# Optimization experiments

Hardware: AMD Instinct MI355X
Metric: run time of the kernel (lower is better)

Reference implementation:

```python
import jax, jax.numpy as jnp
import numpy as np

N, P, K = 2048, 32, 20000

def _log_normal(x, m, s):
    return -0.5 * jnp.log(2.0 * jnp.pi * s * s) - (x - m) ** 2 / (2.0 * s * s)

def setup_inputs() -> dict:
    key = jax.random.key(0)
    k1, k2, k3, k4 = jax.random.split(key, 4)
    X = jax.random.normal(k1, (N, P), dtype=jnp.float32)
    Y = jax.random.randint(k2, (N, K), 0, 100, dtype=jnp.int32)
    mu = jax.random.normal(k3, (K,), dtype=jnp.float32)
    beta = jax.random.normal(k4, (P, K), dtype=jnp.float32)
    m0 = jnp.float32(0.0)
    s0 = jnp.float32(1.0)
    return {"X": X, "Y": Y, "mu": mu, "beta": beta, "m0": m0, "s0": s0}

def reference(X, Y, mu, beta, m0, s0):
    # logits: [N, K]
    logits = mu + jnp.matmul(X, beta)
    # log softmax == log(pi) where pi = exp(logits - logsumexp)
    logp = jax.nn.log_softmax(logits, axis=1)
    Yf = Y.astype(logits.dtype)
    n = jnp.sum(Yf, axis=1)  # total counts per sample
    # sum over samples of multinomial log-pmf:
    #   lgamma(n+1) - sum_j lgamma(y_j+1) + sum_j y_j * log(pi_j)
    log_lik = (jnp.sum(jax.lax.lgamma(n + 1.0))
               - jnp.sum(jax.lax.lgamma(Yf + 1.0))
               + jnp.sum(Yf * logp))
    log_prior = jnp.sum(_log_normal(mu, m0, s0)) + jnp.sum(_log_normal(beta, m0, s0))
    return jnp.reshape(log_lik + log_prior, (1,))
```

## Files before the change

kernel.cpp:

```cpp
#include <hip/hip_runtime.h>
#include <math.h>

#define NROWS 2048
#define KDIM  20000
#define PDIM  32
#define CHW   80
#define SLOTS 20
#define PADW  84
#define KSL   24
#define RGRP  32
#define MAINB (RGRP * KSL)
#define PREPB 313
#define PRIORB 64
#define STATS_N (NROWS * 4)

#define OFF_STATS (KDIM * PDIM * 2)
#define OFF_PRIOR (OFF_STATS + STATS_N * 4)
#define WS_NEEDED (OFF_PRIOR + PREPB * 8)

typedef short bf16x8 __attribute__((ext_vector_type(8)));
typedef unsigned short u16x8 __attribute__((ext_vector_type(8)));
typedef float f32x4  __attribute__((ext_vector_type(4)));
typedef int   i32x4  __attribute__((ext_vector_type(4)));

__device__ __forceinline__ short f2bf(float f) {
  unsigned u = __float_as_uint(f);
  u += 0x7FFF + ((u >> 16) & 1);
  return (short)(u >> 16);
}
__device__ __forceinline__ float wredf(float v) {
#pragma unroll
  for (int o = 32; o > 0; o >>= 1) v += __shfl_down(v, o, 64);
  return v;
}
__device__ __forceinline__ double wredd(double v) {
#pragma unroll
  for (int o = 32; o > 0; o >>= 1) v += __shfl_down(v, o, 64);
  return v;
}


__global__ void prep_k(const float* __restrict__ beta, const float* __restrict__ mu,
                       const float* __restrict__ m0p, const float* __restrict__ s0p,
                       unsigned short* __restrict__ betaT,
                       float* __restrict__ stats, double* __restrict__ priorpart)
{
  __shared__ float red[4];
  const int tid = threadIdx.x;
  const int gi = blockIdx.x * 256 + tid;
  if (gi < STATS_N) stats[gi] = 0.0f;

  const int kk = blockIdx.x * 64 + (tid & 63);
  const int pg = tid >> 6;
  const float m0 = m0p[0], s0 = s0p[0];
  const float inv2s2 = 0.5f / (s0 * s0);
  const float cnst = -0.5f * logf(6.283185307179586f * s0 * s0);

  float fs = 0.0f;
  if (kk < KDIM) {
    u16x8 w;
#pragma unroll
    for (int i = 0; i < 8; ++i) {
      float v = beta[(pg * 8 + i) * KDIM + kk];
      float d = v - m0;
      fs += cnst - d * d * inv2s2;
      w[i] = (unsigned short)f2bf(v);
    }
    *(u16x8*)(betaT + kk * PDIM + pg * 8) = w;
    if (pg == 0) {
      float d = mu[kk] - m0;
      fs += cnst - d * d * inv2s2;
    }
  }
  fs = wredf(fs);
  if ((tid & 63) == 0) red[tid >> 6] = fs;
  __syncthreads();
  if (tid == 0)
    priorpart[blockIdx.x] =
        (double)red[0] + (double)red[1] + (double)red[2] + (double)red[3];
}

__global__ __launch_bounds__(256, 3) void main_k(
    const float* __restrict__ X, const int* __restrict__ Y,
    const float* __restrict__ mu, const unsigned short* __restrict__ betaT,
    float* __restrict__ stats)
{
  __shared__ float lgt[128];
  __shared__ int ybuf[2][64 * PADW];
  const int tid = threadIdx.x;
  if (tid < 128) lgt[tid] = lgammaf((float)tid + 1.0f);

  const int rg = blockIdx.x / KSL;
  const int ks = blockIdx.x % KSL;
  const int sbase = rg * 64;
  const int cstart = (ks < 10) ? ks * 11 : 110 + (ks - 10) * 10;
  const int cps    = (ks < 10) ? 11 : 10;

  const int wave = tid >> 6, lane = tid & 63;
  const int lg = lane >> 4, ln = lane & 15;

  int goff[5], loff[5];
#pragma unroll
  for (int i = 0; i < 5; ++i) {
    const int flat = i * 64 + lane;
    const int rowl = flat / SLOTS, slot = flat % SLOTS;
    const int row = wave * 16 + rowl;
    goff[i] = (sbase + row) * KDIM + slot * 4;
    loff[i] = row * PADW + slot * 4;
  }

  const int samp = sbase + wave * 16 + ln;
  bf16x8 xb;
  {
    const float* xp = X + samp * PDIM + lg * 8;
    float4 x0 = *(const float4*)xp;
    float4 x1 = *(const float4*)(xp + 4);
    xb[0] = f2bf(x0.x); xb[1] = f2bf(x0.y); xb[2] = f2bf(x0.z); xb[3] = f2bf(x0.w);
    xb[4] = f2bf(x1.x); xb[5] = f2bf(x1.y); xb[6] = f2bf(x1.z); xb[7] = f2bf(x1.w);
  }

  float S = 0.f, SY = 0.f, SYL = 0.f, SLG = 0.f;

#define GLOAD(c_) do { const int _cb = (c_) * CHW;                            \
    r0 = *(const i32x4*)(Y + goff[0] + _cb);                                  \
    r1 = *(const i32x4*)(Y + goff[1] + _cb);                                  \
    r2 = *(const i32x4*)(Y + goff[2] + _cb);                                  \
    r3 = *(const i32x4*)(Y + goff[3] + _cb);                                  \
    r4 = *(const i32x4*)(Y + goff[4] + _cb);                                  \
  } while (0)
#define DSW(b_) do {                                                          \
    *(i32x4*)&ybuf[b_][loff[0]] = r0;                                         \
    *(i32x4*)&ybuf[b_][loff[1]] = r1;                                         \
    *(i32x4*)&ybuf[b_][loff[2]] = r2;                                         \
    *(i32x4*)&ybuf[b_][loff[3]] = r3;                                         \
    *(i32x4*)&ybuf[b_][loff[4]] = r4;                                         \
  } while (0)

  i32x4 r0, r1, r2, r3, r4;
  GLOAD(cstart);
  DSW(0);
  GLOAD(cstart + 1);
  __syncthreads();

  const int ybase = wave * 16 + ln;

  for (int ch = 0; ch < cps; ++ch) {
    const int cur = ch & 1;
    const int cbase = (cstart + ch) * CHW;
#pragma unroll
    for (int tt = 0; tt < 5; ++tt) {
      i32x4 yv = *(const i32x4*)&ybuf[cur][ybase * PADW + (tt * 4 + lg) * 4];
      bf16x8 af = *(const bf16x8*)(betaT + (cbase + tt * 16 + ln) * PDIM + lg * 8);
      float4 m4 = *(const float4*)(mu + cbase + tt * 16 + lg * 4);
      f32x4 cc = { m4.x, m4.y, m4.z, m4.w };
      cc = __builtin_amdgcn_mfma_f32_16x16x32_bf16(af, xb, cc, 0, 0, 0);
      const int ya[4] = { yv[0], yv[1], yv[2], yv[3] };
#pragma unroll
      for (int j = 0; j < 4; ++j) {
        const float logit = cc[j];
        S += __expf(logit);
        const float yf = (float)ya[j];
        SY += yf;
        SYL = fmaf(yf, logit, SYL);
        SLG += lgt[ya[j]];
      }
    }
    if (ch + 1 < cps) {
      DSW(cur ^ 1);
      if (ch + 2 < cps) GLOAD(cstart + ch + 2);
    }
  }
#undef GLOAD
#undef DSW

  S   += __shfl_xor(S,   16, 64); S   += __shfl_xor(S,   32, 64);
  SY  += __shfl_xor(SY,  16, 64); SY  += __shfl_xor(SY,  32, 64);
  SYL += __shfl_xor(SYL, 16, 64); SYL += __shfl_xor(SYL, 32, 64);
  SLG += __shfl_xor(SLG, 16, 64); SLG += __shfl_xor(SLG, 32, 64);
  if (lg == 0) {
    atomicAdd(&stats[samp * 4 + 0], S);
    atomicAdd(&stats[samp * 4 + 1], SY);
    atomicAdd(&stats[samp * 4 + 2], SYL);
    atomicAdd(&stats[samp * 4 + 3], SLG);
  }
}

__global__ void combine_k(const float* __restrict__ stats,
                          const double* __restrict__ priorpart,
                          float* __restrict__ out)
{
  double part = 0.0;
  for (int r = threadIdx.x; r < NROWS; r += 256) {
    float S   = stats[r * 4 + 0];
    float n   = stats[r * 4 + 1];
    float SYL = stats[r * 4 + 2];
    float SLG = stats[r * 4 + 3];
    part += (double)lgammaf(n + 1.0f) - (double)SLG + (double)SYL
          - (double)n * (double)logf(S);
  }
  for (int i = threadIdx.x; i < PREPB; i += 256) part += priorpart[i];
  part = wredd(part);
  __shared__ double pd[4];
  if ((threadIdx.x & 63) == 0) pd[threadIdx.x >> 6] = part;
  __syncthreads();
  if (threadIdx.x == 0)
    out[0] = (float)(pd[0] + pd[1] + pd[2] + pd[3]);
}


__global__ void fb_init_k(float* stats, double* acc) {
  int i = blockIdx.x * blockDim.x + threadIdx.x;
  if (i < STATS_N) stats[i] = 0.0f;
  if (i == 0) acc[0] = 0.0;
}

__global__ __launch_bounds__(256, 8) void fb_main_k(
    const float* __restrict__ X, const int* __restrict__ Y,
    const float* __restrict__ mu, const float* __restrict__ beta,
    const float* __restrict__ m0p, const float* __restrict__ s0p,
    float* __restrict__ stats, double* __restrict__ acc)
{
  __shared__ float lgt[128];
  __shared__ float red[4];
  const int tid = threadIdx.x;
  const int FB_MAINB = 2048;

  if (blockIdx.x >= FB_MAINB) {
    const int b = blockIdx.x - FB_MAINB;
    const float m0 = m0p[0], s0 = s0p[0];
    const float inv2s2 = 0.5f / (s0 * s0);
    const float cnst = -0.5f * logf(6.283185307179586f * s0 * s0);
    const int total = KDIM + PDIM * KDIM;
    float fs = 0.0f;
    for (int i = b * 256 + tid; i < total; i += PRIORB * 256) {
      float v = (i < KDIM) ? mu[i] : beta[i - KDIM];
      float d = v - m0;
      fs += cnst - d * d * inv2s2;
    }
    fs = wredf(fs);
    if ((tid & 63) == 0) red[tid >> 6] = fs;
    __syncthreads();
    if (tid == 0) {
      double tsum = (double)red[0] + (double)red[1] + (double)red[2] + (double)red[3];
      atomicAdd(acc, tsum);
    }
    return;
  }

  const int brow  = blockIdx.x / 64;
  const int chunk = blockIdx.x % 64;
  const int wave = tid >> 6;
  const int lane = tid & 63;
  const int lg = lane >> 4;
  const int ln = lane & 15;
  const int sample = brow * 64 + wave * 16 + ln;

  if (tid < 128) lgt[tid] = lgammaf((float)tid + 1.0f);
  __syncthreads();

  bf16x8 xb;
  {
    const float* xp = X + sample * PDIM + lg * 8;
    float4 x0 = *(const float4*)xp;
    float4 x1 = *(const float4*)(xp + 4);
    xb[0] = f2bf(x0.x); xb[1] = f2bf(x0.y); xb[2] = f2bf(x0.z); xb[3] = f2bf(x0.w);
    xb[4] = f2bf(x1.x); xb[5] = f2bf(x1.y); xb[6] = f2bf(x1.z); xb[7] = f2bf(x1.w);
  }
  const size_t ybase = (size_t)sample * KDIM + (size_t)lg * 4;
  const float* bcol = beta + lg * 8 * KDIM + ln;

  float S = 0.f, SY = 0.f, SYL = 0.f, SLG = 0.f;
  int t = chunk;
  const int FB_NTILE = 1250;
  int4   yv = *(const int4*)(Y + ybase + (size_t)t * 16);
  float4 m4 = *(const float4*)(mu + t * 16 + lg * 4);

  while (t < FB_NTILE) {
    const int col0 = t * 16;
    const int tn = t + 64;
    const int ts = (tn < FB_NTILE) ? tn : t;
    int4   yv_n = *(const int4*)(Y + ybase + (size_t)ts * 16);
    float4 m4_n = *(const float4*)(mu + ts * 16 + lg * 4);
    bf16x8 af;
#pragma unroll
    for (int i = 0; i < 8; ++i) af[i] = f2bf(bcol[i * KDIM + col0]);
    f32x4 c = { m4.x, m4.y, m4.z, m4.w };
    c = __builtin_amdgcn_mfma_f32_16x16x32_bf16(af, xb, c, 0, 0, 0);
    const int ya[4] = { yv.x, yv.y, yv.z, yv.w };
#pragma unroll
    for (int j = 0; j < 4; ++j) {
      const float logit = c[j];
      S += __expf(logit);
      const float yf = (float)ya[j];
      SY  += yf;
      SYL += yf * logit;
      SLG += lgt[ya[j]];
    }
    t = tn; yv = yv_n; m4 = m4_n;
  }

  S   += __shfl_xor(S,   16, 64); S   += __shfl_xor(S,   32, 64);
  SY  += __shfl_xor(SY,  16, 64); SY  += __shfl_xor(SY,  32, 64);
  SYL += __shfl_xor(SYL, 16, 64); SYL += __shfl_xor(SYL, 32, 64);
  SLG += __shfl_xor(SLG, 16, 64); SLG += __shfl_xor(SLG, 32, 64);
  if (lg == 0) {
    atomicAdd(&stats[sample * 4 + 0], S);
    atomicAdd(&stats[sample * 4 + 1], SY);
    atomicAdd(&stats[sample * 4 + 2], SYL);
    atomicAdd(&stats[sample * 4 + 3], SLG);
  }
}

__global__ void fb_combine_k(const float* __restrict__ stats,
                             const double* __restrict__ acc,
                             float* __restrict__ out)
{
  double part = 0.0;
  for (int r = threadIdx.x; r < NROWS; r += 256) {
    float S   = stats[r * 4 + 0];
    float n   = stats[r * 4 + 1];
    float SYL = stats[r * 4 + 2];
    float SLG = stats[r * 4 + 3];
    part += (double)lgammaf(n + 1.0f) - (double)SLG + (double)SYL
          - (double)n * (double)logf(S);
  }
  part = wredd(part);
  __shared__ double pd[4];
  if ((threadIdx.x & 63) == 0) pd[threadIdx.x >> 6] = part;
  __syncthreads();
  if (threadIdx.x == 0)
    out[0] = (float)(pd[0] + pd[1] + pd[2] + pd[3] + acc[0]);
}

extern "C" void kernel_launch(void* const* d_in, const int* in_sizes, int n_in,
                              void* d_out, int out_size, void* d_ws, size_t ws_size,
                              hipStream_t stream) {
  const float* X    = (const float*)d_in[0];
  const int*   Y    = (const int*)d_in[1];
  const float* mu   = (const float*)d_in[2];
  const float* beta = (const float*)d_in[3];
  const float* m0   = (const float*)d_in[4];
  const float* s0   = (const float*)d_in[5];
  float* out = (float*)d_out;

  if (ws_size >= (size_t)WS_NEEDED) {
    unsigned short* betaT = (unsigned short*)d_ws;
    float*  stats = (float*)((char*)d_ws + OFF_STATS);
    double* prior = (double*)((char*)d_ws + OFF_PRIOR);
    prep_k<<<dim3(PREPB), dim3(256), 0, stream>>>(beta, mu, m0, s0, betaT, stats, prior);
    main_k<<<dim3(MAINB), dim3(256), 0, stream>>>(X, Y, mu, betaT, stats);
    combine_k<<<dim3(1), dim3(256), 0, stream>>>(stats, prior, out);
  } else {
    float*  stats = (float*)d_ws;
    double* acc   = (double*)((char*)d_ws + STATS_N * sizeof(float));
    fb_init_k<<<dim3((STATS_N + 255) / 256), dim3(256), 0, stream>>>(stats, acc);
    fb_main_k<<<dim3(2048 + PRIORB), dim3(256), 0, stream>>>(
        X, Y, mu, beta, m0, s0, stats, acc);
    fb_combine_k<<<dim3(1), dim3(256), 0, stream>>>(stats, acc, out);
  }
}
```

Measured before the change: 44.84 us.

## Deepen Y prefetch to two register sets and fuse combine via last-block counter

The Y tile loads now use two register sets, so the global load for chunk ch+2 is issued at the start of iteration ch and overlaps a full chunk of MFMA and exp work. Previously it was issued after the LDS store at the end of the iteration. The separate single-block combine kernel is removed: a completion counter reset in prep_k lets the last main_k block do the final reduction, saving one launch. The cost is more live VGPRs, which may hurt occupancy under launch_bounds(256,3), plus a threadfence and an atomic in every block.

Result: slower. 107.1 us (+138.9%).

```diff
diff --git a/kernel.cpp b/kernel.cpp
--- a/kernel.cpp
+++ b/kernel.cpp
@@ -16,7 +16,8 @@
 
 #define OFF_STATS (KDIM * PDIM * 2)
 #define OFF_PRIOR (OFF_STATS + STATS_N * 4)
-#define WS_NEEDED (OFF_PRIOR + PREPB * 8)
+#define OFF_CNT   (OFF_PRIOR + PREPB * 8)
+#define WS_NEEDED (OFF_CNT + 16)
 
 typedef short bf16x8 __attribute__((ext_vector_type(8)));
 typedef unsigned short u16x8 __attribute__((ext_vector_type(8)));
@@ -43,12 +44,14 @@
 __global__ void prep_k(const float* __restrict__ beta, const float* __restrict__ mu,
                        const float* __restrict__ m0p, const float* __restrict__ s0p,
                        unsigned short* __restrict__ betaT,
-                       float* __restrict__ stats, double* __restrict__ priorpart)
+                       float* __restrict__ stats, double* __restrict__ priorpart,
+                       unsigned* __restrict__ counter)
 {
   __shared__ float red[4];
   const int tid = threadIdx.x;
   const int gi = blockIdx.x * 256 + tid;
   if (gi < STATS_N) stats[gi] = 0.0f;
+  if (gi == 0) counter[0] = 0u;
 
   const int kk = blockIdx.x * 64 + (tid & 63);
   const int pg = tid >> 6;
@@ -83,7 +86,8 @@
 __global__ __launch_bounds__(256, 3) void main_k(
     const float* __restrict__ X, const int* __restrict__ Y,
     const float* __restrict__ mu, const unsigned short* __restrict__ betaT,
-    float* __restrict__ stats)
+    float* __restrict__ stats, const double* __restrict__ priorpart,
+    unsigned* __restrict__ counter, float* __restrict__ out)
 {
   __shared__ float lgt[128];
   __shared__ int ybuf[2][64 * PADW];
@@ -121,31 +125,50 @@
 
   float S = 0.f, SY = 0.f, SYL = 0.f, SLG = 0.f;
 
-#define GLOAD(c_) do { const int _cb = (c_) * CHW;                            \
-    r0 = *(const i32x4*)(Y + goff[0] + _cb);                                  \
-    r1 = *(const i32x4*)(Y + goff[1] + _cb);                                  \
-    r2 = *(const i32x4*)(Y + goff[2] + _cb);                                  \
-    r3 = *(const i32x4*)(Y + goff[3] + _cb);                                  \
-    r4 = *(const i32x4*)(Y + goff[4] + _cb);                                  \
+  i32x4 rA0, rA1, rA2, rA3, rA4;
+  i32x4 rB0, rB1, rB2, rB3, rB4;
+#define GLOADA(c_) do { const int _cb = (c_) * CHW;                           \
+    rA0 = *(const i32x4*)(Y + goff[0] + _cb);                                 \
+    rA1 = *(const i32x4*)(Y + goff[1] + _cb);                                 \
+    rA2 = *(const i32x4*)(Y + goff[2] + _cb);                                 \
+    rA3 = *(const i32x4*)(Y + goff[3] + _cb);                                 \
+    rA4 = *(const i32x4*)(Y + goff[4] + _cb);                                 \
   } while (0)
-#define DSW(b_) do {                                                          \
-    *(i32x4*)&ybuf[b_][loff[0]] = r0;                                         \
-    *(i32x4*)&ybuf[b_][loff[1]] = r1;                                         \
-    *(i32x4*)&ybuf[b_][loff[2]] = r2;                                         \
-    *(i32x4*)&ybuf[b_][loff[3]] = r3;                                         \
-    *(i32x4*)&ybuf[b_][loff[4]] = r4;                                         \
+#define GLOADB(c_) do { const int _cb = (c_) * CHW;                           \
+    rB0 = *(const i32x4*)(Y + goff[0] + _cb);                                 \
+    rB1 = *(const i32x4*)(Y + goff[1] + _cb);                                 \
+    rB2 = *(const i32x4*)(Y + goff[2] + _cb);                                 \
+    rB3 = *(const i32x4*)(Y + goff[3] + _cb);                                 \
+    rB4 = *(const i32x4*)(Y + goff[4] + _cb);                                 \
   } while (0)
-
-  i32x4 r0, r1, r2, r3, r4;
-  GLOAD(cstart);
-  DSW(0);
-  GLOAD(cstart + 1);
+#define DSWA(b_) do {                                                         \
+    *(i32x4*)&ybuf[b_][loff[0]] = rA0;                                        \
+    *(i32x4*)&ybuf[b_][loff[1]] = rA1;                                        \
+    *(i32x4*)&ybuf[b_][loff[2]] = rA2;                                        \
+    *(i32x4*)&ybuf[b_][loff[3]] = rA3;                                        \
+    *(i32x4*)&ybuf[b_][loff[4]] = rA4;                                        \
+  } while (0)
+#define DSWB(b_) do {                                                         \
+    *(i32x4*)&ybuf[b_][loff[0]] = rB0;                                        \
+    *(i32x4*)&ybuf[b_][loff[1]] = rB1;                                        \
+    *(i32x4*)&ybuf[b_][loff[2]] = rB2;                                        \
+    *(i32x4*)&ybuf[b_][loff[3]] = rB3;                                        \
+    *(i32x4*)&ybuf[b_][loff[4]] = rB4;                                        \
+  } while (0)
+
+  GLOADA(cstart);
+  GLOADB(cstart + 1);
+  DSWA(0);
   __syncthreads();
 
   const int ybase = wave * 16 + ln;
 
   for (int ch = 0; ch < cps; ++ch) {
     const int cur = ch & 1;
+    if (ch + 2 < cps) {
+      if (cur == 0) GLOADA(cstart + ch + 2);
+      else          GLOADB(cstart + ch + 2);
+    }
     const int cbase = (cstart + ch) * CHW;
 #pragma unroll
     for (int tt = 0; tt < 5; ++tt) {
@@ -166,12 +189,14 @@
       }
     }
     if (ch + 1 < cps) {
-      DSW(cur ^ 1);
-      if (ch + 2 < cps) GLOAD(cstart + ch + 2);
-    }
-  }
-#undef GLOAD
-#undef DSW
+      if (cur == 0) DSWB(cur ^ 1);
+      else          DSWA(cur ^ 1);
+    }
+  }
+#undef GLOADA
+#undef GLOADB
+#undef DSWA
+#undef DSWB
 
   S   += __shfl_xor(S,   16, 64); S   += __shfl_xor(S,   32, 64);
   SY  += __shfl_xor(SY,  16, 64); SY  += __shfl_xor(SY,  32, 64);
@@ -183,28 +208,32 @@
     atomicAdd(&stats[samp * 4 + 2], SYL);
     atomicAdd(&stats[samp * 4 + 3], SLG);
   }
-}
-
-__global__ void combine_k(const float* __restrict__ stats,
-                          const double* __restrict__ priorpart,
-                          float* __restrict__ out)
-{
-  double part = 0.0;
-  for (int r = threadIdx.x; r < NROWS; r += 256) {
-    float S   = stats[r * 4 + 0];
-    float n   = stats[r * 4 + 1];
-    float SYL = stats[r * 4 + 2];
-    float SLG = stats[r * 4 + 3];
-    part += (double)lgammaf(n + 1.0f) - (double)SLG + (double)SYL
-          - (double)n * (double)logf(S);
-  }
-  for (int i = threadIdx.x; i < PREPB; i += 256) part += priorpart[i];
-  part = wredd(part);
-  __shared__ double pd[4];
-  if ((threadIdx.x & 63) == 0) pd[threadIdx.x >> 6] = part;
-  __syncthreads();
-  if (threadIdx.x == 0)
-    out[0] = (float)(pd[0] + pd[1] + pd[2] + pd[3]);
+
+  __threadfence();
+  __shared__ unsigned lastflag;
+  if (tid == 0) {
+    unsigned old = atomicAdd(counter, 1u);
+    lastflag = (old == (unsigned)(MAINB - 1)) ? 1u : 0u;
+  }
+  __syncthreads();
+  if (lastflag) {
+    double part = 0.0;
+    for (int r = tid; r < NROWS; r += 256) {
+      float Sv  = __hip_atomic_load(&stats[r * 4 + 0], __ATOMIC_RELAXED, __HIP_MEMORY_SCOPE_AGENT);
+      float nv  = __hip_atomic_load(&stats[r * 4 + 1], __ATOMIC_RELAXED, __HIP_MEMORY_SCOPE_AGENT);
+      float SYLv= __hip_atomic_load(&stats[r * 4 + 2], __ATOMIC_RELAXED, __HIP_MEMORY_SCOPE_AGENT);
+      float SLGv= __hip_atomic_load(&stats[r * 4 + 3], __ATOMIC_RELAXED, __HIP_MEMORY_SCOPE_AGENT);
+      part += (double)lgammaf(nv + 1.0f) - (double)SLGv + (double)SYLv
+            - (double)nv * (double)logf(Sv);
+    }
+    for (int i = tid; i < PREPB; i += 256) part += priorpart[i];
+    part = wredd(part);
+    __shared__ double pd[4];
+    if ((tid & 63) == 0) pd[tid >> 6] = part;
+    __syncthreads();
+    if (tid == 0)
+      out[0] = (float)(pd[0] + pd[1] + pd[2] + pd[3]);
+  }
 }
 
 
@@ -347,9 +376,9 @@
     unsigned short* betaT = (unsigned short*)d_ws;
     float*  stats = (float*)((char*)d_ws + OFF_STATS);
     double* prior = (double*)((char*)d_ws + OFF_PRIOR);
-    prep_k<<<dim3(PREPB), dim3(256), 0, stream>>>(beta, mu, m0, s0, betaT, stats, prior);
-    main_k<<<dim3(MAINB), dim3(256), 0, stream>>>(X, Y, mu, betaT, stats);
-    combine_k<<<dim3(1), dim3(256), 0, stream>>>(stats, prior, out);
+    unsigned* cnt = (unsigned*)((char*)d_ws + OFF_CNT);
+    prep_k<<<dim3(PREPB), dim3(256), 0, stream>>>(beta, mu, m0, s0, betaT, stats, prior, cnt);
+    main_k<<<dim3(MAINB), dim3(256), 0, stream>>>(X, Y, mu, betaT, stats, prior, cnt, out);
   } else {
     float*  stats = (float*)d_ws;
     double* acc   = (double*)((char*)d_ws + STATS_N * sizeof(float));
```
